# Kernel optimization log

Measured on AMD Instinct MI355X. Metric: run time of the kernel, lower is better.

## Reference

```python
import jax, jax.numpy as jnp
import numpy as np

N_VERTS = 100000
N_JOINTS = 24
N_BETAS = 10
N_POSEDIRS = 207  # (24-1)*9
# Standard SMPL kinematic tree parents
PARENTS = np.array([-1, 0, 0, 0, 1, 2, 3, 4, 5, 6, 7, 8, 9, 9, 9, 12, 13, 14, 16, 17, 18, 19, 20, 21])


def setup_inputs() -> dict:
    key = jax.random.key(0)
    ks = jax.random.split(key, 9)
    f = jnp.float32
    return {
        "betas": jax.random.normal(ks[0], (N_BETAS,), f),
        "pose": jax.random.normal(ks[1], (N_JOINTS, 3), f) * 0.2,
        "scale": jnp.ones((1,), f),
        "trans": jax.random.normal(ks[2], (3,), f),
        "v_template": jax.random.normal(ks[3], (N_VERTS, 3), f),
        "shapedirs": jax.random.normal(ks[4], (N_VERTS, 3, N_BETAS), f) * 0.01,
        "posedirs": jax.random.normal(ks[5], (N_VERTS, 3, N_POSEDIRS), f) * 0.01,
        "J_regressor": jax.random.uniform(ks[6], (N_JOINTS, N_VERTS), f) / N_VERTS,
        "weights": jax.nn.softmax(jax.random.normal(ks[7], (N_VERTS, N_JOINTS), f), axis=-1),
    }


def rodrigues(r):
    """Axis-angle [J,3] -> rotation matrices [J,3,3] (matches torch impl; eps kept tiny+deterministic)."""
    theta = jnp.linalg.norm(r + 1e-8, axis=-1, keepdims=True)  # [J,1]
    r_hat = r / theta
    z = jnp.zeros_like(r_hat[:, 0])
    K = jnp.stack([z, -r_hat[:, 2], r_hat[:, 1],
                   r_hat[:, 2], z, -r_hat[:, 0],
                   -r_hat[:, 1], r_hat[:, 0], z], axis=1).reshape(-1, 3, 3)
    c = jnp.cos(theta)[..., None]  # [J,1,1]
    s = jnp.sin(theta)[..., None]
    outer = r_hat[:, :, None] * r_hat[:, None, :]  # [J,3,3]
    I = jnp.eye(3, dtype=r.dtype)
    return c * I + (1.0 - c) * outer + s * K


def reference(betas, pose, scale, trans, v_template, shapedirs, posedirs, J_regressor, weights):
    dt = v_template.dtype
    # blend shapes
    v_shaped = jnp.einsum('vks,s->vk', shapedirs, betas) + v_template  # [V,3]
    J = J_regressor @ v_shaped  # [24,3]
    R = rodrigues(pose)  # [24,3,3]
    I3 = jnp.eye(3, dtype=dt)
    lrotmin = (R[1:] - I3).reshape(-1)  # [207]
    v_posed = v_shaped + jnp.einsum('vkp,p->vk', posedirs, lrotmin)  # [V,3]
    # forward kinematics over 24-joint chain
    bottom = jnp.array([[0.0, 0.0, 0.0, 1.0]], dtype=dt)
    def make_A(Ri, t):
        return jnp.concatenate([jnp.concatenate([Ri, t[:, None]], axis=1), bottom], axis=0)  # [4,4]
    As = [make_A(R[0], J[0])]
    for i in range(1, N_JOINTS):
        p = int(PARENTS[i])
        As.append(As[p] @ make_A(R[i], J[i] - J[p]))
    G = jnp.stack(As)  # [24,4,4]
    # remove rest-pose joint locations
    Jh = jnp.concatenate([J, jnp.zeros((N_JOINTS, 1), dt)], axis=1)  # [24,4]
    corr = jnp.einsum('jab,jb->ja', G, Jh)  # [24,4]
    rel = G - jnp.concatenate([jnp.zeros((N_JOINTS, 4, 3), dt), corr[:, :, None]], axis=2)
    # linear blend skinning
    T = jnp.einsum('vj,jab->vab', weights, rel)  # [V,4,4]
    vh = jnp.concatenate([v_posed, jnp.ones((v_posed.shape[0], 1), dt)], axis=1)  # [V,4]
    v = jnp.einsum('vab,vb->va', T, vh)[:, :3]  # [V,3]
    return v * scale.reshape(()) + trans[None, :]
```

## Files before the change

### kernel.cpp

```cpp
#include <hip/hip_runtime.h>

#define NV 100000
#define NJ 24
#define NP 207
#define NPART 25
#define NPAIRS (NV / 2)
#define GRIDF 1024
#define NWV (GRIDF * 4)

__device__ __forceinline__ float dpp_red32(float x) {
  x += __int_as_float(__builtin_amdgcn_update_dpp(0, __float_as_int(x), 0x111, 0xf, 0xf, true));
  x += __int_as_float(__builtin_amdgcn_update_dpp(0, __float_as_int(x), 0x112, 0xf, 0xf, true));
  x += __int_as_float(__builtin_amdgcn_update_dpp(0, __float_as_int(x), 0x114, 0xf, 0xf, true));
  x += __int_as_float(__builtin_amdgcn_update_dpp(0, __float_as_int(x), 0x118, 0xf, 0xf, true));
  x += __int_as_float(__builtin_amdgcn_update_dpp(0, __float_as_int(x), 0x142, 0xf, 0xf, true));
  return x;
}

__global__ __launch_bounds__(256) void k_shape(
    const float* __restrict__ betas, const float* __restrict__ v_template,
    const float* __restrict__ shapedirs, float* __restrict__ v_shaped) {
  __shared__ float sb[10];
  if (threadIdx.x < 10) sb[threadIdx.x] = betas[threadIdx.x];
  __syncthreads();
  int t = blockIdx.x * 256 + threadIdx.x;
  if (t >= 3 * NV / 2) return;
  const float4* sd4 = (const float4*)(shapedirs + (size_t)t * 20);
  float4 f0 = sd4[0], f1 = sd4[1], f2 = sd4[2], f3 = sd4[3], f4v = sd4[4];
  float2 vt = ((const float2*)v_template)[t];
  float a = vt.x
          + f0.x * sb[0] + f0.y * sb[1] + f0.z * sb[2] + f0.w * sb[3]
          + f1.x * sb[4] + f1.y * sb[5] + f1.z * sb[6] + f1.w * sb[7]
          + f2.x * sb[8] + f2.y * sb[9];
  float b = vt.y
          + f2.z * sb[0] + f2.w * sb[1]
          + f3.x * sb[2] + f3.y * sb[3] + f3.z * sb[4] + f3.w * sb[5]
          + f4v.x * sb[6] + f4v.y * sb[7] + f4v.z * sb[8] + f4v.w * sb[9];
  ((float2*)v_shaped)[t] = make_float2(a, b);
}

__global__ __launch_bounds__(256) void k_jreg(
    const float* __restrict__ Jreg, const float* __restrict__ v_shaped,
    float* __restrict__ jpT) {
  int j = blockIdx.x, part = blockIdx.y, tid = threadIdx.x;
  const int SL = NV / NPART;
  int v0 = part * SL;
  const float4* w4 = (const float4*)(Jreg + (size_t)j * NV + v0);
  const float4* s4 = (const float4*)(v_shaped + (size_t)3 * v0);
  float s0 = 0.f, s1 = 0.f, s2 = 0.f;
  for (int i4 = tid; i4 < SL / 4; i4 += 256) {
    float4 w = w4[i4];
    float4 A = s4[3 * i4 + 0];
    float4 B = s4[3 * i4 + 1];
    float4 C = s4[3 * i4 + 2];
    s0 += w.x * A.x + w.y * A.w + w.z * B.z + w.w * C.y;
    s1 += w.x * A.y + w.y * B.x + w.z * B.w + w.w * C.z;
    s2 += w.x * A.z + w.y * B.y + w.z * C.x + w.w * C.w;
  }
  __shared__ float red[256][3];
  red[tid][0] = s0; red[tid][1] = s1; red[tid][2] = s2;
  __syncthreads();
  for (int off = 128; off > 0; off >>= 1) {
    if (tid < off) {
      red[tid][0] += red[tid + off][0];
      red[tid][1] += red[tid + off][1];
      red[tid][2] += red[tid + off][2];
    }
    __syncthreads();
  }
  if (tid < 3) jpT[(j * 3 + tid) * 32 + part] = red[0][tid];
}

__device__ __forceinline__ void stage_pair(float4* dst, const float4* src, int lane) {
  #pragma unroll
  for (int r = 0; r < 5; ++r) {
    int i4 = r * 64 + lane;
    int i4c = (i4 < 311) ? i4 : 310;
    __builtin_amdgcn_global_load_lds(
        (const __attribute__((address_space(1))) void*)(src + i4c),
        (__attribute__((address_space(3))) void*)(dst + r * 64),
        16, 0, 0);
  }
}

__device__ __forceinline__ const float4* pair_src(const float* posedirs, int p) {
  size_t startf = (size_t)1242 * p - ((p & 1) ? 2 : 0);
  return (const float4*)(posedirs + startf);
}

__global__ __launch_bounds__(256, 4) void k_fused(
    const float* __restrict__ posedirs, const float* __restrict__ wgt,
    const float* __restrict__ pose, const float* __restrict__ jpT,
    const float* __restrict__ scale, const float* __restrict__ trans,
    float* __restrict__ vbuf) {
  __shared__ float4 buf[4][2][320];
  int tid = threadIdx.x, b = blockIdx.x;
  int wid = tid >> 6, lane = tid & 63, half = lane >> 5, lj = lane & 31;
  int W = b * 4 + wid;
  int sh = (W & 1) ? 2 : 0;

  float pvl = (lj < 3) ? vbuf[(size_t)3 * (W * 2 + half) + lj] : 0.f;
  float wj  = (lj < NJ) ? wgt[(size_t)(W * 2 + half) * NJ + lj] : 0.f;
  __builtin_amdgcn_sched_barrier(0);
  stage_pair(&buf[wid][0][0], pair_src(posedirs, W), lane);

  float* fkJ  = (float*)&buf[0][1][0];
  float* fkR  = fkJ + 72;
  float* fkG  = fkJ + 288;
  float* lrs  = fkJ + 576;
  float* relS = fkJ + 784;
  if (tid < NJ * 3) {
    const float* src = jpT + tid * 32;
    float a = 0.f;
    #pragma unroll
    for (int i = 0; i < NPART; ++i) a += src[i];
    fkJ[tid] = a;
  }
  if (tid < NJ) {
    float rx = pose[tid * 3 + 0], ry = pose[tid * 3 + 1], rz = pose[tid * 3 + 2];
    float tx = rx + 1e-8f, ty = ry + 1e-8f, tz = rz + 1e-8f;
    float theta = sqrtf(tx * tx + ty * ty + tz * tz);
    float x = rx / theta, y = ry / theta, z = rz / theta;
    float c = cosf(theta), s = sinf(theta), C = 1.f - c;
    float Rr[9];
    Rr[0] = c + C * x * x;     Rr[1] = C * x * y - s * z; Rr[2] = C * x * z + s * y;
    Rr[3] = C * x * y + s * z; Rr[4] = c + C * y * y;     Rr[5] = C * y * z - s * x;
    Rr[6] = C * x * z - s * y; Rr[7] = C * y * z + s * x; Rr[8] = c + C * z * z;
    #pragma unroll
    for (int e = 0; e < 9; ++e) fkR[tid * 9 + e] = Rr[e];
    if (tid >= 1) {
      #pragma unroll
      for (int e = 0; e < 9; ++e) {
        float id = (e == 0 || e == 4 || e == 8) ? 1.f : 0.f;
        lrs[(tid - 1) * 9 + e] = Rr[e] - id;
      }
    }
  }
  __syncthreads();
  if (tid < 3) {
    const int par[NJ] = {-1,0,0,0,1,2,3,4,5,6,7,8,9,9,9,12,13,14,16,17,18,19,20,21};
    int a = tid;
    fkG[a * 4 + 0] = fkR[a * 3 + 0];
    fkG[a * 4 + 1] = fkR[a * 3 + 1];
    fkG[a * 4 + 2] = fkR[a * 3 + 2];
    fkG[a * 4 + 3] = fkJ[a];
    #pragma unroll
    for (int i = 1; i < NJ; ++i) {
      int p = par[i];
      float t0 = fkJ[i * 3 + 0] - fkJ[p * 3 + 0];
      float t1 = fkJ[i * 3 + 1] - fkJ[p * 3 + 1];
      float t2 = fkJ[i * 3 + 2] - fkJ[p * 3 + 2];
      float g0 = fkG[p * 12 + a * 4 + 0], g1 = fkG[p * 12 + a * 4 + 1];
      float g2 = fkG[p * 12 + a * 4 + 2], g3 = fkG[p * 12 + a * 4 + 3];
      fkG[i * 12 + a * 4 + 0] = g0 * fkR[i * 9 + 0] + g1 * fkR[i * 9 + 3] + g2 * fkR[i * 9 + 6];
      fkG[i * 12 + a * 4 + 1] = g0 * fkR[i * 9 + 1] + g1 * fkR[i * 9 + 4] + g2 * fkR[i * 9 + 7];
      fkG[i * 12 + a * 4 + 2] = g0 * fkR[i * 9 + 2] + g1 * fkR[i * 9 + 5] + g2 * fkR[i * 9 + 8];
      fkG[i * 12 + a * 4 + 3] = g3 + g0 * t0 + g1 * t1 + g2 * t2;
    }
  }
  __syncthreads();
  if (tid < NJ) {
    #pragma unroll
    for (int a = 0; a < 3; ++a) {
      float corr = fkG[tid * 12 + a * 4 + 0] * fkJ[tid * 3 + 0] +
                   fkG[tid * 12 + a * 4 + 1] * fkJ[tid * 3 + 1] +
                   fkG[tid * 12 + a * 4 + 2] * fkJ[tid * 3 + 2];
      relS[tid * 12 + a * 4 + 0] = fkG[tid * 12 + a * 4 + 0];
      relS[tid * 12 + a * 4 + 1] = fkG[tid * 12 + a * 4 + 1];
      relS[tid * 12 + a * 4 + 2] = fkG[tid * 12 + a * 4 + 2];
      relS[tid * 12 + a * 4 + 3] = fkG[tid * 12 + a * 4 + 3] - corr;
    }
  }
  __syncthreads();

  float llr[7];
  #pragma unroll
  for (int e = 0; e < 7; ++e) {
    int p = lj + 32 * e;
    llr[e] = (p < NP) ? lrs[p] : 0.f;
  }
  float rlq[12];
  #pragma unroll
  for (int e = 0; e < 12; ++e) rlq[e] = (lj < NJ) ? relS[lj * 12 + e] : 0.f;
  float sc = scale[0];
  float tr = (lj < 3) ? trans[lj] : 0.f;

  __syncthreads();
  asm volatile("s_waitcnt vmcnt(0)" ::: "memory");

  int nt = (NPAIRS - 1 - W) / NWV + 1;
  for (int it = 0; it < nt; ++it) {
    int cur = it & 1;
    int pn = W + (it + 1) * NWV;
    if (pn >= NPAIRS) pn = NPAIRS - 1;
    float pvl_n = (lj < 3) ? vbuf[(size_t)3 * (pn * 2 + half) + lj] : 0.f;
    float wj_n  = (lj < NJ) ? wgt[(size_t)(pn * 2 + half) * NJ + lj] : 0.f;
    __builtin_amdgcn_sched_barrier(0);
    stage_pair(&buf[wid][cur ^ 1][0], pair_src(posedirs, pn), lane);
    asm volatile("s_waitcnt vmcnt(7)" ::: "memory");
    __builtin_amdgcn_sched_barrier(0);

    int p = W + it * NWV;
    int vv = p * 2 + half;
    const float* row = (const float*)&buf[wid][cur][0] + sh + half * (3 * NP);
    float a0 = 0.f, a1 = 0.f, a2 = 0.f;
    #pragma unroll
    for (int e = 0; e < 7; ++e) {
      int pp = lj + 32 * e;
      if (pp < NP) {
        float l = llr[e];
        a0 += row[pp] * l;
        a1 += row[NP + pp] * l;
        a2 += row[2 * NP + pp] * l;
      }
    }
    int gb = lane & 32;
    a0 = __shfl(dpp_red32(a0), gb + 31);
    a1 = __shfl(dpp_red32(a1), gb + 31);
    a2 = __shfl(dpp_red32(a2), gb + 31);
    float p0 = __shfl(pvl, gb + 0) + a0;
    float p1 = __shfl(pvl, gb + 1) + a1;
    float p2 = __shfl(pvl, gb + 2) + a2;
    float q0v = rlq[0] * p0 + rlq[1] * p1 + rlq[2]  * p2 + rlq[3];
    float q1v = rlq[4] * p0 + rlq[5] * p1 + rlq[6]  * p2 + rlq[7];
    float q2v = rlq[8] * p0 + rlq[9] * p1 + rlq[10] * p2 + rlq[11];
    float r0 = __shfl(dpp_red32(wj * q0v), gb + 31);
    float r1 = __shfl(dpp_red32(wj * q1v), gb + 31);
    float r2 = __shfl(dpp_red32(wj * q2v), gb + 31);
    if (lj < 3) {
      float oo = (lj == 0) ? r0 : (lj == 1) ? r1 : r2;
      vbuf[(size_t)3 * vv + lj] = oo * sc + tr;
    }
    pvl = pvl_n; wj = wj_n;
  }
  asm volatile("s_waitcnt vmcnt(0)" ::: "memory");
}

extern "C" void kernel_launch(void* const* d_in, const int* in_sizes, int n_in,
                              void* d_out, int out_size, void* d_ws, size_t ws_size,
                              hipStream_t stream) {
  const float* betas      = (const float*)d_in[0];
  const float* pose       = (const float*)d_in[1];
  const float* scale      = (const float*)d_in[2];
  const float* trans      = (const float*)d_in[3];
  const float* v_template = (const float*)d_in[4];
  const float* shapedirs  = (const float*)d_in[5];
  const float* posedirs   = (const float*)d_in[6];
  const float* Jreg       = (const float*)d_in[7];
  const float* weights    = (const float*)d_in[8];
  float* out = (float*)d_out;
  float* ws  = (float*)d_ws;

  float* jpT = ws;

  k_shape<<<(3 * NV / 2 + 255) / 256, 256, 0, stream>>>(betas, v_template, shapedirs, out);
  k_jreg<<<dim3(NJ, NPART), 256, 0, stream>>>(Jreg, out, jpT);
  k_fused<<<GRIDF, 256, 0, stream>>>(posedirs, weights, pose, jpT, scale, trans, out);
}
```

Measured before the change: 58.36 us.

## Map one vertex per wavefront instead of two per half-wave

```diff
diff --git a/kernel.cpp b/kernel.cpp
--- a/kernel.cpp
+++ b/kernel.cpp
@@ -4,16 +4,16 @@
 #define NJ 24
 #define NP 207
 #define NPART 25
-#define NPAIRS (NV / 2)
-#define GRIDF 1024
+#define GRIDF 2048
 #define NWV (GRIDF * 4)
 
-__device__ __forceinline__ float dpp_red32(float x) {
+__device__ __forceinline__ float dpp_red64(float x) {
   x += __int_as_float(__builtin_amdgcn_update_dpp(0, __float_as_int(x), 0x111, 0xf, 0xf, true));
   x += __int_as_float(__builtin_amdgcn_update_dpp(0, __float_as_int(x), 0x112, 0xf, 0xf, true));
   x += __int_as_float(__builtin_amdgcn_update_dpp(0, __float_as_int(x), 0x114, 0xf, 0xf, true));
   x += __int_as_float(__builtin_amdgcn_update_dpp(0, __float_as_int(x), 0x118, 0xf, 0xf, true));
   x += __int_as_float(__builtin_amdgcn_update_dpp(0, __float_as_int(x), 0x142, 0xf, 0xf, true));
+  x += __int_as_float(__builtin_amdgcn_update_dpp(0, __float_as_int(x), 0x143, 0xf, 0xf, true));
   return x;
 }
 
@@ -71,44 +71,46 @@
   if (tid < 3) jpT[(j * 3 + tid) * 32 + part] = red[0][tid];
 }
 
-__device__ __forceinline__ void stage_pair(float4* dst, const float4* src, int lane) {
-  #pragma unroll
-  for (int r = 0; r < 5; ++r) {
-    int i4 = r * 64 + lane;
-    int i4c = (i4 < 311) ? i4 : 310;
+__device__ __forceinline__ void stage_vert(float4* dst, const float4* src, int lane) {
+  __builtin_amdgcn_global_load_lds(
+      (const __attribute__((address_space(1))) void*)(src + lane),
+      (__attribute__((address_space(3))) void*)(dst), 16, 0, 0);
+  __builtin_amdgcn_global_load_lds(
+      (const __attribute__((address_space(1))) void*)(src + 64 + lane),
+      (__attribute__((address_space(3))) void*)(dst + 64), 16, 0, 0);
+  if (lane < 28) {
     __builtin_amdgcn_global_load_lds(
-        (const __attribute__((address_space(1))) void*)(src + i4c),
-        (__attribute__((address_space(3))) void*)(dst + r * 64),
-        16, 0, 0);
-  }
-}
-
-__device__ __forceinline__ const float4* pair_src(const float* posedirs, int p) {
-  size_t startf = (size_t)1242 * p - ((p & 1) ? 2 : 0);
-  return (const float4*)(posedirs + startf);
-}
-
-__global__ __launch_bounds__(256, 4) void k_fused(
+        (const __attribute__((address_space(1))) void*)(src + 128 + lane),
+        (__attribute__((address_space(3))) void*)(dst + 128), 16, 0, 0);
+  }
+}
+
+__device__ __forceinline__ const float4* vert_src(const float* posedirs, int v) {
+  size_t startf = (size_t)1863 * v / 3;
+  return (const float4*)(posedirs + ((size_t)621 * v - (v & 3)));
+}
+
+__global__ __launch_bounds__(256, 8) void k_fused(
     const float* __restrict__ posedirs, const float* __restrict__ wgt,
     const float* __restrict__ pose, const float* __restrict__ jpT,
     const float* __restrict__ scale, const float* __restrict__ trans,
     float* __restrict__ vbuf) {
-  __shared__ float4 buf[4][2][320];
+  __shared__ float4 buf[4][2][160];
   int tid = threadIdx.x, b = blockIdx.x;
-  int wid = tid >> 6, lane = tid & 63, half = lane >> 5, lj = lane & 31;
+  int wid = tid >> 6, lane = tid & 63;
   int W = b * 4 + wid;
-  int sh = (W & 1) ? 2 : 0;
-
-  float pvl = (lj < 3) ? vbuf[(size_t)3 * (W * 2 + half) + lj] : 0.f;
-  float wj  = (lj < NJ) ? wgt[(size_t)(W * 2 + half) * NJ + lj] : 0.f;
+  int sh = W & 3;
+
+  float pvl = (lane < 3) ? vbuf[(size_t)3 * W + lane] : 0.f;
+  float wj  = (lane < NJ) ? wgt[(size_t)W * NJ + lane] : 0.f;
   __builtin_amdgcn_sched_barrier(0);
-  stage_pair(&buf[wid][0][0], pair_src(posedirs, W), lane);
+  stage_vert(&buf[wid][0][0], vert_src(posedirs, W), lane);
 
   float* fkJ  = (float*)&buf[0][1][0];
   float* fkR  = fkJ + 72;
-  float* fkG  = fkJ + 288;
-  float* lrs  = fkJ + 576;
-  float* relS = fkJ + 784;
+  float* lrs  = fkJ + 288;
+  float* fkG  = (float*)&buf[1][1][0];
+  float* relS = fkG + 288;
   if (tid < NJ * 3) {
     const float* src = jpT + tid * 32;
     float a = 0.f;
@@ -173,63 +175,61 @@
   }
   __syncthreads();
 
-  float llr[7];
+  float llr[4];
   #pragma unroll
-  for (int e = 0; e < 7; ++e) {
-    int p = lj + 32 * e;
+  for (int e = 0; e < 4; ++e) {
+    int p = lane + 64 * e;
     llr[e] = (p < NP) ? lrs[p] : 0.f;
   }
   float rlq[12];
   #pragma unroll
-  for (int e = 0; e < 12; ++e) rlq[e] = (lj < NJ) ? relS[lj * 12 + e] : 0.f;
+  for (int e = 0; e < 12; ++e) rlq[e] = (lane < NJ) ? relS[lane * 12 + e] : 0.f;
   float sc = scale[0];
-  float tr = (lj < 3) ? trans[lj] : 0.f;
+  float tr = (lane < 3) ? trans[lane] : 0.f;
 
   __syncthreads();
   asm volatile("s_waitcnt vmcnt(0)" ::: "memory");
 
-  int nt = (NPAIRS - 1 - W) / NWV + 1;
+  int nt = (NV - 1 - W) / NWV + 1;
   for (int it = 0; it < nt; ++it) {
     int cur = it & 1;
-    int pn = W + (it + 1) * NWV;
-    if (pn >= NPAIRS) pn = NPAIRS - 1;
-    float pvl_n = (lj < 3) ? vbuf[(size_t)3 * (pn * 2 + half) + lj] : 0.f;
-    float wj_n  = (lj < NJ) ? wgt[(size_t)(pn * 2 + half) * NJ + lj] : 0.f;
+    int vn = W + (it + 1) * NWV;
+    if (vn >= NV) vn = NV - 1;
+    float pvl_n = (lane < 3) ? vbuf[(size_t)3 * vn + lane] : 0.f;
+    float wj_n  = (lane < NJ) ? wgt[(size_t)vn * NJ + lane] : 0.f;
     __builtin_amdgcn_sched_barrier(0);
-    stage_pair(&buf[wid][cur ^ 1][0], pair_src(posedirs, pn), lane);
-    asm volatile("s_waitcnt vmcnt(7)" ::: "memory");
+    stage_vert(&buf[wid][cur ^ 1][0], vert_src(posedirs, vn), lane);
+    asm volatile("s_waitcnt vmcnt(5)" ::: "memory");
     __builtin_amdgcn_sched_barrier(0);
 
-    int p = W + it * NWV;
-    int vv = p * 2 + half;
-    const float* row = (const float*)&buf[wid][cur][0] + sh + half * (3 * NP);
+    int v = W + it * NWV;
+    const float* row = (const float*)&buf[wid][cur][0] + sh;
     float a0 = 0.f, a1 = 0.f, a2 = 0.f;
     #pragma unroll
-    for (int e = 0; e < 7; ++e) {
-      int pp = lj + 32 * e;
-      if (pp < NP) {
+    for (int e = 0; e < 4; ++e) {
+      int p = lane + 64 * e;
+      if (p < NP) {
         float l = llr[e];
-        a0 += row[pp] * l;
-        a1 += row[NP + pp] * l;
-        a2 += row[2 * NP + pp] * l;
+        a0 += row[p] * l;
+        a1 += row[NP + p] * l;
+        a2 += row[2 * NP + p] * l;
       }
     }
-    int gb = lane & 32;
-    a0 = __shfl(dpp_red32(a0), gb + 31);
-    a1 = __shfl(dpp_red32(a1), gb + 31);
-    a2 = __shfl(dpp_red32(a2), gb + 31);
-    float p0 = __shfl(pvl, gb + 0) + a0;
-    float p1 = __shfl(pvl, gb + 1) + a1;
-    float p2 = __shfl(pvl, gb + 2) + a2;
+    a0 = __shfl(dpp_red64(a0), 63);
+    a1 = __shfl(dpp_red64(a1), 63);
+    a2 = __shfl(dpp_red64(a2), 63);
+    float p0 = __shfl(pvl, 0) + a0;
+    float p1 = __shfl(pvl, 1) + a1;
+    float p2 = __shfl(pvl, 2) + a2;
     float q0v = rlq[0] * p0 + rlq[1] * p1 + rlq[2]  * p2 + rlq[3];
     float q1v = rlq[4] * p0 + rlq[5] * p1 + rlq[6]  * p2 + rlq[7];
     float q2v = rlq[8] * p0 + rlq[9] * p1 + rlq[10] * p2 + rlq[11];
-    float r0 = __shfl(dpp_red32(wj * q0v), gb + 31);
-    float r1 = __shfl(dpp_red32(wj * q1v), gb + 31);
-    float r2 = __shfl(dpp_red32(wj * q2v), gb + 31);
-    if (lj < 3) {
-      float oo = (lj == 0) ? r0 : (lj == 1) ? r1 : r2;
-      vbuf[(size_t)3 * vv + lj] = oo * sc + tr;
+    float r0 = __shfl(dpp_red64(wj * q0v), 63);
+    float r1 = __shfl(dpp_red64(wj * q1v), 63);
+    float r2 = __shfl(dpp_red64(wj * q2v), 63);
+    if (lane < 3) {
+      float oo = (lane == 0) ? r0 : (lane == 1) ? r1 : r2;
+      vbuf[(size_t)3 * v + lane] = oo * sc + tr;
     }
     pvl = pvl_n; wj = wj_n;
   }
```

After: 59.99 us. 2.8% more time.
